# Optimization experiments

Hardware: AMD Instinct MI355X
Metric: run time of the kernel (lower is better)

The kernel has to match this reference:

```python
import jax, jax.numpy as jnp
import numpy as np

EPS = 1e-5
NUM_HEADS = 8

def _bn(x, w, b, m, v):
    # inference-mode BatchNorm2d over channel dim of (B,C,H,W)
    inv = w / jnp.sqrt(v + EPS)
    return x * inv[None, :, None, None] + (b - m * inv)[None, :, None, None]

def _conv1x1(x, W, b):
    # 1x1 conv == per-pixel matmul: W is (out_ch, in_ch)
    return jnp.einsum('bchw,ec->behw', x, W) + b[None, :, None, None]

def _forward(x, bn1_w, bn1_b, bn1_m, bn1_v, Wq, bq, Wk, bk, Wv, bv, gamma, temperature,
             conv_w, conv_b, cbn_w, cbn_b, cbn_m, cbn_v, rs_w, rs_b, rbn_w, rbn_b, rbn_m, rbn_v):
    B, C, Wd, Hd = x.shape
    S = Wd * Hd
    E = Wq.shape[0]
    hd = E // NUM_HEADS
    xa = jax.nn.relu(_bn(x, bn1_w, bn1_b, bn1_m, bn1_v))
    def proj(Wm, bm):
        return _conv1x1(xa, Wm, bm).reshape(B, NUM_HEADS, hd, S).transpose(0, 1, 3, 2)  # (B,h,S,d)
    q = proj(Wq, bq)
    k = proj(Wk, bk)
    v = proj(Wv, bv)
    scores = jnp.einsum('bhsd,bhtd->bhst', q, k) / temperature  # (B,h,S,S)
    scores = scores - jnp.max(scores, axis=-1, keepdims=True)   # redundant amax-subtract as in source
    attn = jax.nn.softmax(scores, axis=-1)
    out = jnp.einsum('bhst,bhtd->bhsd', attn, v)
    out = out.transpose(0, 1, 3, 2).reshape(B, E, Wd, Hd)
    conv_path = jax.nn.relu(_bn(_conv1x1(x, conv_w, conv_b), cbn_w, cbn_b, cbn_m, cbn_v))
    fused = gamma[0] * out + conv_path
    return jax.nn.gelu(_bn(_conv1x1(fused, rs_w, rs_b), rbn_w, rbn_b, rbn_m, rbn_v), approximate=False)

def setup_inputs() -> dict:
    key = jax.random.key(0)
    ks = jax.random.split(key, 18)
    C, E = 256, 512
    n = lambda k, s, sc=0.02: jax.random.normal(k, s, jnp.float32) * sc
    return {
        'x': jax.random.normal(ks[0], (1, C, 64, 64), jnp.float32),
        'bn1_w': 1.0 + n(ks[1], (C,), 0.1), 'bn1_b': n(ks[2], (C,), 0.1),
        'bn1_m': n(ks[3], (C,), 0.05), 'bn1_v': 0.5 + jax.random.uniform(ks[4], (C,), jnp.float32),
        'Wq': n(ks[5], (E, C)), 'bq': jnp.zeros((E,), jnp.float32),
        'Wk': n(ks[6], (E, C)), 'bk': jnp.zeros((E,), jnp.float32),
        'Wv': n(ks[7], (E, C)), 'bv': jnp.zeros((E,), jnp.float32),
        'gamma': jnp.full((1,), 0.5, jnp.float32),
        'temperature': jnp.asarray(0.85, jnp.float32),
        'conv_w': n(ks[8], (E, C)), 'conv_b': jnp.zeros((E,), jnp.float32),
        'cbn_w': 1.0 + n(ks[9], (E,), 0.1), 'cbn_b': n(ks[10], (E,), 0.1),
        'cbn_m': n(ks[11], (E,), 0.05), 'cbn_v': 0.5 + jax.random.uniform(ks[12], (E,), jnp.float32),
        'rs_w': n(ks[13], (C, E)), 'rs_b': jnp.zeros((C,), jnp.float32),
        'rbn_w': 1.0 + n(ks[14], (C,), 0.1), 'rbn_b': n(ks[15], (C,), 0.1),
        'rbn_m': n(ks[16], (C,), 0.05), 'rbn_v': 0.5 + jax.random.uniform(ks[17], (C,), jnp.float32),
    }

def reference(x, bn1_w, bn1_b, bn1_m, bn1_v, Wq, bq, Wk, bk, Wv, bv, gamma, temperature,
              conv_w, conv_b, cbn_w, cbn_b, cbn_m, cbn_v, rs_w, rs_b, rbn_w, rbn_b, rbn_m, rbn_v):
    return _forward(x, bn1_w, bn1_b, bn1_m, bn1_v, Wq, bq, Wk, bk, Wv, bv, gamma, temperature,
                    conv_w, conv_b, cbn_w, cbn_b, cbn_m, cbn_v, rs_w, rs_b, rbn_w, rbn_b, rbn_m, rbn_v)
```

## Files before the change

### kernel.cpp

```cpp
#include <hip/hip_runtime.h>

#define S_DIM 4096
#define C_IN  256
#define E_DIM 512
#define HD    64
#define EPSV  1e-5f

typedef __attribute__((ext_vector_type(8))) short s8v;
typedef __attribute__((ext_vector_type(4))) short s4v;
typedef __attribute__((ext_vector_type(4))) float f4v;
typedef __attribute__((ext_vector_type(16))) float f16v;

__device__ __forceinline__ float bf2f(unsigned short h){
  union{unsigned u; float f;} v; v.u = ((unsigned)h)<<16; return v.f;
}
__device__ __forceinline__ unsigned short f2bf(float f){
  union{float f; unsigned u;} v; v.f = f;
  unsigned r = v.u + 0x7fffu + ((v.u>>16)&1u);
  return (unsigned short)(r>>16);
}
__device__ __forceinline__ unsigned cvtpk_bf16(float lo, float hi_){
  unsigned r;
  asm("v_cvt_pk_bf16_f32 %0, %1, %2" : "=v"(r) : "v"(lo), "v"(hi_));
  return r;
}
__device__ __forceinline__ s8v lds_rd8(const unsigned short* b, int row, int ck){
  return *(const s8v*)&b[(row<<6) + (((ck)^(row&7))<<3)];
}
__device__ __forceinline__ void lds_wr8(unsigned short* b, int row, int ck, s8v v){
  *(s8v*)&b[(row<<6) + (((ck)^(row&7))<<3)] = v;
}
__device__ __forceinline__ s4v lds_rd4q(const unsigned short* b, int row, int q4){
  return *(const s4v*)&b[(row<<6) + (((q4)^(row&15))<<2)];
}
__device__ __forceinline__ void gl_lds16(const unsigned short* g, unsigned short* l){
  __builtin_amdgcn_global_load_lds(
      (const __attribute__((address_space(1))) unsigned int*)g,
      (__attribute__((address_space(3))) unsigned int*)l, 16, 0, 0);
}

__global__ __launch_bounds__(256) void k_wcvt(const float* __restrict__ w0,
    const float* __restrict__ w1, const float* __restrict__ w2,
    const float* __restrict__ w3, const float* __restrict__ w4,
    unsigned short* __restrict__ dst){
  int i = blockIdx.x*256 + threadIdx.x;
  int z = blockIdx.y;
  const float* s = (z==0)?w0:(z==1)?w1:(z==2)?w2:(z==3)?w3:w4;
  dst[z*(E_DIM*C_IN) + i] = f2bf(s[i]);
}

__global__ __launch_bounds__(256) void k_prep(const float* __restrict__ x,
    const float* __restrict__ bw, const float* __restrict__ bb,
    const float* __restrict__ bm, const float* __restrict__ bvar,
    unsigned short* __restrict__ XaT, unsigned short* __restrict__ XrT){
  __shared__ float tile[32][33];
  int tid = threadIdx.x;
  int tx = tid & 31, ty = tid >> 5;
  int s0 = blockIdx.x*32, c0 = blockIdx.y*32;
  #pragma unroll
  for(int p=0;p<4;p++){
    int c = c0 + ty + p*8;
    tile[ty+p*8][tx] = x[c*S_DIM + s0 + tx];
  }
  __syncthreads();
  int cc = c0 + tx;
  float inv  = bw[cc] * rsqrtf(bvar[cc] + EPSV);
  float beta = bb[cc] - bm[cc]*inv;
  #pragma unroll
  for(int p=0;p<4;p++){
    int s = s0 + ty + p*8;
    float v = tile[tx][ty+p*8];
    float a = v*inv + beta; a = a>0.f?a:0.f;
    XaT[s*C_IN + cc] = f2bf(a);
    XrT[s*C_IN + cc] = f2bf(v);
  }
}

__global__ __launch_bounds__(256) void k_proj(
    const unsigned short* __restrict__ XaT, const unsigned short* __restrict__ XrT,
    const unsigned short* __restrict__ Wb,
    const float* __restrict__ bq, const float* __restrict__ bk,
    const float* __restrict__ bvb, const float* __restrict__ bc,
    const float* __restrict__ cw, const float* __restrict__ cbb,
    const float* __restrict__ cm, const float* __restrict__ cvv,
    unsigned short* __restrict__ QT, unsigned short* __restrict__ KT,
    unsigned short* __restrict__ Vx, unsigned short* __restrict__ CT){
  int z = blockIdx.z;
  const unsigned short* Xin = (z==3) ? XrT : XaT;
  const unsigned short* W   = Wb + z*(E_DIM*C_IN);
  const float* bias = (z==0)?bq:(z==1)?bk:(z==2)?bvb:bc;

  __shared__ unsigned short Als[128*64];
  __shared__ unsigned short Bls[64*64];
  int tid = threadIdx.x;
  int w = tid>>6, l = tid&63, g = l>>4, c16 = l&15;
  int wr = w>>1, wc = w&1;
  int s0 = blockIdx.x*128, e0 = blockIdx.y*64;

  f4v acc[4][2];
  #pragma unroll
  for(int m=0;m<4;m++)
    #pragma unroll
    for(int n=0;n<2;n++) acc[m][n] = (f4v){0.f,0.f,0.f,0.f};

  for(int kk=0;kk<4;kk++){
    __syncthreads();
    #pragma unroll
    for(int p=0;p<4;p++){
      int ck = p*256 + tid, row = ck>>3, ch = ck&7;
      s8v v = *(const s8v*)&Xin[(s0+row)*C_IN + kk*64 + ch*8];
      lds_wr8(Als, row, ch, v);
    }
    #pragma unroll
    for(int p=0;p<2;p++){
      int ck = p*256 + tid, row = ck>>3, ch = ck&7;
      s8v v = *(const s8v*)&W[(e0+row)*C_IN + kk*64 + ch*8];
      lds_wr8(Bls, row, ch, v);
    }
    __syncthreads();
    #pragma unroll
    for(int kb=0;kb<2;kb++){
      s8v bfr[2];
      #pragma unroll
      for(int n=0;n<2;n++) bfr[n] = lds_rd8(Bls, wc*32 + n*16 + c16, g + kb*4);
      #pragma unroll
      for(int m=0;m<4;m++){
        s8v af = lds_rd8(Als, wr*64 + m*16 + c16, g + kb*4);
        #pragma unroll
        for(int n=0;n<2;n++)
          acc[m][n] = __builtin_amdgcn_mfma_f32_16x16x32_bf16(af, bfr[n], acc[m][n], 0,0,0);
      }
    }
  }
  #pragma unroll
  for(int n=0;n<2;n++){
    int e = e0 + wc*32 + n*16 + c16;
    float bsv = bias[e];
    float cinv = 0.f, cbeta = 0.f;
    if(z==3){ cinv = cw[e]*rsqrtf(cvv[e]+EPSV); cbeta = cbb[e] - cm[e]*cinv; }
    #pragma unroll
    for(int m=0;m<4;m++){
      int sb = s0 + wr*64 + m*16 + g*4;
      if(z==2){
        s4v pk;
        #pragma unroll
        for(int i=0;i<4;i++) pk[i] = (short)f2bf(acc[m][n][i] + bsv);
        int sb2 = (sb & ~63) | ((((sb>>2)&15) ^ (e&15))<<2);
        *(s4v*)&Vx[e*S_DIM + sb2] = pk;
      } else {
        unsigned short* dst = (z==0)?QT:(z==1)?KT:CT;
        #pragma unroll
        for(int i=0;i<4;i++){
          float vv = acc[m][n][i] + bsv;
          if(z==3){ vv = vv*cinv + cbeta; vv = vv>0.f?vv:0.f; }
          int key = sb+i;
          int ee = e;
          if(z==1) ee = (e & ~56) | ((((e>>3)&7) ^ (key&7))<<3);
          dst[key*E_DIM + ee] = f2bf(vv);
        }
      }
    }
  }
}

__global__ __launch_bounds__(512,2) void k_attn(
    const unsigned short* __restrict__ QT, const unsigned short* __restrict__ KT,
    const unsigned short* __restrict__ Vx, const unsigned short* __restrict__ CT,
    const float* __restrict__ gamma, const float* __restrict__ temp,
    unsigned short* __restrict__ fusedT){
  __shared__ unsigned short SM[65536];
  int tid = threadIdx.x;
  int w = tid>>6, l = tid&63, l31 = l&31, hi = l>>5;
  int qh = w>>2, kh = w&3;
  int bx = blockIdx.x;
  int h = bx&7;
  int q0b = (bx>>3)*128;
  float scl = 1.4426950408889634f / temp[0];

  s8v qf[2][4];
  #pragma unroll
  for(int qg=0;qg<2;qg++){
    int q = q0b + qh*64 + qg*32 + l31;
    #pragma unroll
    for(int ks=0;ks<4;ks++){
      s8v r = *(const s8v*)&QT[q*E_DIM + h*HD + ks*16 + hi*8];
      #pragma unroll
      for(int j=0;j<8;j++) qf[qg][ks][j] = (short)f2bf(bf2f((unsigned short)r[j])*scl);
    }
  }
  s8v ones;
  #pragma unroll
  for(int j=0;j<8;j++) ones[j] = (short)0x3F80;

  f16v oacc[2][2];
  f16v lacc[2];
  #pragma unroll
  for(int qg=0;qg<2;qg++){
    #pragma unroll
    for(int r=0;r<16;r++){ oacc[qg][0][r]=0.f; oacc[qg][1][r]=0.f; lacc[qg][r]=0.f; }
  }

  #define STAGE(BUF, T) { \
    _Pragma("unroll") \
    for(int j=0;j<8;j++){ \
      int flat = (w*8+j)*64 + l; \
      int tile = flat>>9, gg = flat&511, row = gg>>3, ch = gg&7; \
      int khp = tile&3; \
      int sK = khp*1024 + (T)*64; \
      const unsigned short* src = (tile<4) \
        ? &KT[(sK+row)*E_DIM + h*HD + ch*8] \
        : &Vx[(h*HD+row)*S_DIM + sK + ch*8]; \
      gl_lds16(src, SM + (BUF)*32768 + (w*8+j)*512); \
    } }

  int buf = 0;
  STAGE(0, 0);
  for(int t=0;t<16;t++){
    asm volatile("s_waitcnt vmcnt(0)" ::: "memory");
    __syncthreads();
    if(t<15) STAGE(buf^1, t+1);
    const unsigned short* Kb = SM + buf*32768 + kh*4096;
    const unsigned short* Vb = SM + buf*32768 + (4+kh)*4096;

    #pragma unroll
    for(int sub=0;sub<2;sub++){
      int kr = sub*32 + l31;
      s8v kf[4];
      #pragma unroll
      for(int ks=0;ks<4;ks++) kf[ks] = lds_rd8(Kb, kr, ks*2 + hi);

      union{ s8v v; unsigned u[4]; } pa[2][2];
      #pragma unroll
      for(int qg=0;qg<2;qg++){
        f16v d;
        #pragma unroll
        for(int r=0;r<16;r++) d[r]=0.f;
        #pragma unroll
        for(int ks=0;ks<4;ks++)
          d = __builtin_amdgcn_mfma_f32_32x32x16_bf16(kf[ks], qf[qg][ks], d, 0,0,0);
        float e_[16];
        #pragma unroll
        for(int r=0;r<16;r++) e_[r] = __builtin_amdgcn_exp2f(d[r]);
        #pragma unroll
        for(int j=0;j<4;j++){
          pa[qg][0].u[j] = cvtpk_bf16(e_[2*j],   e_[2*j+1]);
          pa[qg][1].u[j] = cvtpk_bf16(e_[8+2*j], e_[8+2*j+1]);
        }
        lacc[qg] = __builtin_amdgcn_mfma_f32_32x32x16_bf16(pa[qg][0].v, ones, lacc[qg],0,0,0);
        lacc[qg] = __builtin_amdgcn_mfma_f32_32x32x16_bf16(pa[qg][1].v, ones, lacc[qg],0,0,0);
      }
      #pragma unroll
      for(int dt=0;dt<2;dt++){
        int vr = dt*32 + l31;
        union{ s8v v; s4v h2[2]; } vf;
        vf.h2[0] = lds_rd4q(Vb, vr, sub*8 + hi);
        vf.h2[1] = lds_rd4q(Vb, vr, sub*8 + 2 + hi);
        oacc[0][dt] = __builtin_amdgcn_mfma_f32_32x32x16_bf16(pa[0][0].v, vf.v, oacc[0][dt], 0,0,0);
        oacc[1][dt] = __builtin_amdgcn_mfma_f32_32x32x16_bf16(pa[1][0].v, vf.v, oacc[1][dt], 0,0,0);
        vf.h2[0] = lds_rd4q(Vb, vr, sub*8 + 4 + hi);
        vf.h2[1] = lds_rd4q(Vb, vr, sub*8 + 6 + hi);
        oacc[0][dt] = __builtin_amdgcn_mfma_f32_32x32x16_bf16(pa[0][1].v, vf.v, oacc[0][dt], 0,0,0);
        oacc[1][dt] = __builtin_amdgcn_mfma_f32_32x32x16_bf16(pa[1][1].v, vf.v, oacc[1][dt], 0,0,0);
      }
    }
    buf ^= 1;
  }

  float* slab = (float*)SM;
  float ga = gamma[0];
  #pragma unroll
  for(int qg=0;qg<2;qg++){
    __syncthreads();
    if(kh!=0){
      float* dst = slab + ((qh*3 + (kh-1))*64 + l)*48;
      #pragma unroll
      for(int r=0;r<16;r++){
        dst[r] = oacc[qg][0][r]; dst[16+r] = oacc[qg][1][r]; dst[32+r] = lacc[qg][r];
      }
    }
    __syncthreads();
    if(kh==0){
      f16v o0 = oacc[qg][0], o1 = oacc[qg][1], lt = lacc[qg];
      #pragma unroll
      for(int s=0;s<3;s++){
        const float* src = slab + ((qh*3 + s)*64 + l)*48;
        #pragma unroll
        for(int r=0;r<16;r++){ o0[r] += src[r]; o1[r] += src[16+r]; lt[r] += src[32+r]; }
      }
      #pragma unroll
      for(int r=0;r<16;r++){
        int qrow = q0b + qh*64 + qg*32 + (r&3) + 8*(r>>2) + 4*hi;
        float rl = __builtin_amdgcn_rcpf(lt[r]) * ga;
        int e0i = h*HD + l31;
        float oA = o0[r]*rl + bf2f(CT[qrow*E_DIM + e0i]);
        float oB = o1[r]*rl + bf2f(CT[qrow*E_DIM + e0i + 32]);
        fusedT[qrow*E_DIM + e0i]      = f2bf(oA);
        fusedT[qrow*E_DIM + e0i + 32] = f2bf(oB);
      }
    }
  }
  #undef STAGE
}

__global__ __launch_bounds__(256) void k_final(
    const unsigned short* __restrict__ Wrs,
    const unsigned short* __restrict__ fusedT,
    const float* __restrict__ rsb,
    const float* __restrict__ rw, const float* __restrict__ rbb,
    const float* __restrict__ rm, const float* __restrict__ rv,
    float* __restrict__ out){
  __shared__ unsigned short Als[64*64];
  __shared__ unsigned short Bls[64*64];
  int tid = threadIdx.x;
  int w = tid>>6, l = tid&63, g = l>>4, c16 = l&15;
  int wr2 = w>>1, wc2 = w&1;
  int sB0 = blockIdx.x*64, c0 = blockIdx.y*64;
  f4v acc[2][2];
  #pragma unroll
  for(int m=0;m<2;m++)
    #pragma unroll
    for(int n=0;n<2;n++) acc[m][n]=(f4v){0.f,0.f,0.f,0.f};
  for(int kk=0;kk<8;kk++){
    __syncthreads();
    #pragma unroll
    for(int p=0;p<2;p++){
      int ck = p*256+tid, row=ck>>3, ch=ck&7;
      s8v v = *(const s8v*)&Wrs[(c0+row)*E_DIM + kk*64 + ch*8];
      lds_wr8(Als, row, ch, v);
    }
    #pragma unroll
    for(int p=0;p<2;p++){
      int ck = p*256+tid, row=ck>>3, ch=ck&7;
      s8v v = *(const s8v*)&fusedT[(sB0+row)*E_DIM + kk*64 + ch*8];
      lds_wr8(Bls, row, ch, v);
    }
    __syncthreads();
    #pragma unroll
    for(int kb=0;kb<2;kb++){
      s8v af[2]; s8v bfr[2];
      #pragma unroll
      for(int m=0;m<2;m++) af[m] = lds_rd8(Als, wr2*32 + m*16 + c16, g + kb*4);
      #pragma unroll
      for(int n=0;n<2;n++) bfr[n] = lds_rd8(Bls, wc2*32 + n*16 + c16, g + kb*4);
      #pragma unroll
      for(int m=0;m<2;m++)
        #pragma unroll
        for(int n=0;n<2;n++)
          acc[m][n] = __builtin_amdgcn_mfma_f32_16x16x32_bf16(af[m], bfr[n], acc[m][n],0,0,0);
    }
  }
  #pragma unroll
  for(int m=0;m<2;m++){
    #pragma unroll
    for(int i=0;i<4;i++){
      int c = c0 + wr2*32 + m*16 + g*4 + i;
      float bias = rsb[c];
      float rinv = rw[c]*rsqrtf(rv[c]+EPSV);
      float rbeta = rbb[c] - rm[c]*rinv;
      #pragma unroll
      for(int n=0;n<2;n++){
        int s = sB0 + wc2*32 + n*16 + c16;
        float vv = acc[m][n][i] + bias;
        vv = vv*rinv + rbeta;
        out[c*S_DIM + s] = 0.5f*vv*(1.0f + erff(vv*0.70710678118f));
      }
    }
  }
}

extern "C" void kernel_launch(void* const* d_in, const int* in_sizes, int n_in,
                              void* d_out, int out_size, void* d_ws, size_t ws_size,
                              hipStream_t stream){
  const float* x     = (const float*)d_in[0];
  const float* bn1w  = (const float*)d_in[1];
  const float* bn1b  = (const float*)d_in[2];
  const float* bn1m  = (const float*)d_in[3];
  const float* bn1v  = (const float*)d_in[4];
  const float* Wq    = (const float*)d_in[5];
  const float* bq    = (const float*)d_in[6];
  const float* Wk    = (const float*)d_in[7];
  const float* bk    = (const float*)d_in[8];
  const float* Wv    = (const float*)d_in[9];
  const float* bv    = (const float*)d_in[10];
  const float* gamma = (const float*)d_in[11];
  const float* temp  = (const float*)d_in[12];
  const float* convw = (const float*)d_in[13];
  const float* convb = (const float*)d_in[14];
  const float* cbnw  = (const float*)d_in[15];
  const float* cbnb  = (const float*)d_in[16];
  const float* cbnm  = (const float*)d_in[17];
  const float* cbnv  = (const float*)d_in[18];
  const float* rsw   = (const float*)d_in[19];
  const float* rsbp  = (const float*)d_in[20];
  const float* rbnw  = (const float*)d_in[21];
  const float* rbnb  = (const float*)d_in[22];
  const float* rbnm  = (const float*)d_in[23];
  const float* rbnv  = (const float*)d_in[24];
  float* out = (float*)d_out;

  unsigned short* ws  = (unsigned short*)d_ws;
  unsigned short* XaT = ws;
  unsigned short* XrT = XaT + S_DIM*C_IN;
  unsigned short* Wb  = XrT + S_DIM*C_IN;
  unsigned short* Wrs = Wb + 4*E_DIM*C_IN;
  unsigned short* QT  = Wrs + C_IN*E_DIM;
  unsigned short* KT  = QT + S_DIM*E_DIM;
  unsigned short* Vx  = KT + S_DIM*E_DIM;
  unsigned short* CT  = Vx + S_DIM*E_DIM;
  unsigned short* fusedT = CT + S_DIM*E_DIM;

  k_wcvt<<<dim3(512,5),256,0,stream>>>(Wq, Wk, Wv, convw, rsw, Wb);
  k_prep<<<dim3(128,8),256,0,stream>>>(x, bn1w, bn1b, bn1m, bn1v, XaT, XrT);
  k_proj<<<dim3(32,8,4),256,0,stream>>>(XaT, XrT, Wb, bq, bk, bv, convb,
                                        cbnw, cbnb, cbnm, cbnv, QT, KT, Vx, CT);
  k_attn<<<dim3(256),512,0,stream>>>(QT, KT, Vx, CT, gamma, temp, fusedT);
  k_final<<<dim3(64,4),256,0,stream>>>(Wrs, fusedT, rsbp, rbnw, rbnb, rbnm, rbnv, out);
}
```

Measured before the change: 87.96 us.

## Split K/V staging, replace ones-MFMA row sums with scalar sums, add setprio

The attention kernel now stages K and V tiles in separate phases with partial vmcnt waits. The next K tile loads while QK^T and exp run, and the next V tile loads while PV runs. The softmax denominator is no longer computed by extra MFMAs against a ones vector; each lane sums its exp values and the sums are combined with a cross-half shuffle and a shared LDS buffer in the epilogue. s_setprio is placed around the MFMA sections. This removes some matrix-core work and exposed load latency, but adds a second barrier per iteration and more complex epilogue indexing, which risks a correctness error in the row-sum mapping.

Result: no change. 88.89 us (+1.1%).

```diff
diff --git a/kernel.cpp b/kernel.cpp
--- a/kernel.cpp
+++ b/kernel.cpp
@@ -177,6 +177,26 @@
   int q0b = (bx>>3)*128;
   float scl = 1.4426950408889634f / temp[0];
 
+  #define STAGE_K(BUF, T) { \
+    _Pragma("unroll") \
+    for(int j=0;j<4;j++){ \
+      int c = w*4 + j; int flat = c*64 + l; \
+      int tile = flat>>9, gg = flat&511, row = gg>>3, ch = gg&7; \
+      int sK = tile*1024 + (T)*64; \
+      gl_lds16(&KT[(sK+row)*E_DIM + h*HD + ch*8], SM + (BUF)*32768 + c*512); \
+    } }
+  #define STAGE_V(BUF, T) { \
+    _Pragma("unroll") \
+    for(int j=0;j<4;j++){ \
+      int c = 32 + w*4 + j; int flat = c*64 + l; \
+      int tile = (flat>>9)&3, gg = flat&511, row = gg>>3, ch = gg&7; \
+      int sK = tile*1024 + (T)*64; \
+      gl_lds16(&Vx[(h*HD+row)*S_DIM + sK + ch*8], SM + (BUF)*32768 + c*512); \
+    } }
+
+  STAGE_K(0, 0);
+  STAGE_V(0, 0);
+
   s8v qf[2][4];
   #pragma unroll
   for(int qg=0;qg<2;qg++){
@@ -188,118 +208,130 @@
       for(int j=0;j<8;j++) qf[qg][ks][j] = (short)f2bf(bf2f((unsigned short)r[j])*scl);
     }
   }
-  s8v ones;
-  #pragma unroll
-  for(int j=0;j<8;j++) ones[j] = (short)0x3F80;
 
   f16v oacc[2][2];
-  f16v lacc[2];
-  #pragma unroll
-  for(int qg=0;qg<2;qg++){
-    #pragma unroll
-    for(int r=0;r<16;r++){ oacc[qg][0][r]=0.f; oacc[qg][1][r]=0.f; lacc[qg][r]=0.f; }
-  }
-
-  #define STAGE(BUF, T) { \
-    _Pragma("unroll") \
-    for(int j=0;j<8;j++){ \
-      int flat = (w*8+j)*64 + l; \
-      int tile = flat>>9, gg = flat&511, row = gg>>3, ch = gg&7; \
-      int khp = tile&3; \
-      int sK = khp*1024 + (T)*64; \
-      const unsigned short* src = (tile<4) \
-        ? &KT[(sK+row)*E_DIM + h*HD + ch*8] \
-        : &Vx[(h*HD+row)*S_DIM + sK + ch*8]; \
-      gl_lds16(src, SM + (BUF)*32768 + (w*8+j)*512); \
-    } }
+  #pragma unroll
+  for(int qg=0;qg<2;qg++)
+    #pragma unroll
+    for(int dt=0;dt<2;dt++)
+      #pragma unroll
+      for(int r=0;r<16;r++) oacc[qg][dt][r]=0.f;
+  float lrun[2] = {0.f, 0.f};
 
   int buf = 0;
-  STAGE(0, 0);
+  #pragma unroll 1
   for(int t=0;t<16;t++){
-    asm volatile("s_waitcnt vmcnt(0)" ::: "memory");
-    __syncthreads();
-    if(t<15) STAGE(buf^1, t+1);
+    asm volatile("s_waitcnt vmcnt(4)" ::: "memory");
+    __builtin_amdgcn_s_barrier();
+    if(t<15) STAGE_K(buf^1, t+1);
     const unsigned short* Kb = SM + buf*32768 + kh*4096;
-    const unsigned short* Vb = SM + buf*32768 + (4+kh)*4096;
-
+
+    union{ s8v v; unsigned u[4]; } pa[2][2][2];
     #pragma unroll
     for(int sub=0;sub<2;sub++){
       int kr = sub*32 + l31;
       s8v kf[4];
       #pragma unroll
       for(int ks=0;ks<4;ks++) kf[ks] = lds_rd8(Kb, kr, ks*2 + hi);
-
-      union{ s8v v; unsigned u[4]; } pa[2][2];
       #pragma unroll
       for(int qg=0;qg<2;qg++){
         f16v d;
         #pragma unroll
         for(int r=0;r<16;r++) d[r]=0.f;
+        __builtin_amdgcn_s_setprio(1);
         #pragma unroll
         for(int ks=0;ks<4;ks++)
           d = __builtin_amdgcn_mfma_f32_32x32x16_bf16(kf[ks], qf[qg][ks], d, 0,0,0);
-        float e_[16];
-        #pragma unroll
-        for(int r=0;r<16;r++) e_[r] = __builtin_amdgcn_exp2f(d[r]);
+        __builtin_amdgcn_s_setprio(0);
+        float e_[16], ls = 0.f;
+        #pragma unroll
+        for(int r=0;r<16;r++){ e_[r] = __builtin_amdgcn_exp2f(d[r]); ls += e_[r]; }
+        lrun[qg] += ls;
         #pragma unroll
         for(int j=0;j<4;j++){
-          pa[qg][0].u[j] = cvtpk_bf16(e_[2*j],   e_[2*j+1]);
-          pa[qg][1].u[j] = cvtpk_bf16(e_[8+2*j], e_[8+2*j+1]);
+          pa[sub][qg][0].u[j] = cvtpk_bf16(e_[2*j],   e_[2*j+1]);
+          pa[sub][qg][1].u[j] = cvtpk_bf16(e_[8+2*j], e_[8+2*j+1]);
         }
-        lacc[qg] = __builtin_amdgcn_mfma_f32_32x32x16_bf16(pa[qg][0].v, ones, lacc[qg],0,0,0);
-        lacc[qg] = __builtin_amdgcn_mfma_f32_32x32x16_bf16(pa[qg][1].v, ones, lacc[qg],0,0,0);
-      }
+      }
+    }
+
+    if(t<15){ asm volatile("s_waitcnt vmcnt(4)" ::: "memory"); }
+    else    { asm volatile("s_waitcnt vmcnt(0)" ::: "memory"); }
+    __builtin_amdgcn_s_barrier();
+    if(t<15) STAGE_V(buf^1, t+1);
+    const unsigned short* Vb = SM + buf*32768 + (4+kh)*4096;
+
+    __builtin_amdgcn_s_setprio(1);
+    #pragma unroll
+    for(int sub=0;sub<2;sub++){
       #pragma unroll
       for(int dt=0;dt<2;dt++){
         int vr = dt*32 + l31;
         union{ s8v v; s4v h2[2]; } vf;
         vf.h2[0] = lds_rd4q(Vb, vr, sub*8 + hi);
         vf.h2[1] = lds_rd4q(Vb, vr, sub*8 + 2 + hi);
-        oacc[0][dt] = __builtin_amdgcn_mfma_f32_32x32x16_bf16(pa[0][0].v, vf.v, oacc[0][dt], 0,0,0);
-        oacc[1][dt] = __builtin_amdgcn_mfma_f32_32x32x16_bf16(pa[1][0].v, vf.v, oacc[1][dt], 0,0,0);
+        oacc[0][dt] = __builtin_amdgcn_mfma_f32_32x32x16_bf16(pa[sub][0][0].v, vf.v, oacc[0][dt], 0,0,0);
+        oacc[1][dt] = __builtin_amdgcn_mfma_f32_32x32x16_bf16(pa[sub][1][0].v, vf.v, oacc[1][dt], 0,0,0);
         vf.h2[0] = lds_rd4q(Vb, vr, sub*8 + 4 + hi);
         vf.h2[1] = lds_rd4q(Vb, vr, sub*8 + 6 + hi);
-        oacc[0][dt] = __builtin_amdgcn_mfma_f32_32x32x16_bf16(pa[0][1].v, vf.v, oacc[0][dt], 0,0,0);
-        oacc[1][dt] = __builtin_amdgcn_mfma_f32_32x32x16_bf16(pa[1][1].v, vf.v, oacc[1][dt], 0,0,0);
-      }
-    }
+        oacc[0][dt] = __builtin_amdgcn_mfma_f32_32x32x16_bf16(pa[sub][0][1].v, vf.v, oacc[0][dt], 0,0,0);
+        oacc[1][dt] = __builtin_amdgcn_mfma_f32_32x32x16_bf16(pa[sub][1][1].v, vf.v, oacc[1][dt], 0,0,0);
+      }
+    }
+    __builtin_amdgcn_s_setprio(0);
     buf ^= 1;
   }
 
+  #pragma unroll
+  for(int qg=0;qg<2;qg++) lrun[qg] += __shfl_xor(lrun[qg], 32);
+
   float* slab = (float*)SM;
+  float* l_buf = slab + 6*64*33;
   float ga = gamma[0];
   #pragma unroll
   for(int qg=0;qg<2;qg++){
     __syncthreads();
     if(kh!=0){
-      float* dst = slab + ((qh*3 + (kh-1))*64 + l)*48;
-      #pragma unroll
-      for(int r=0;r<16;r++){
-        dst[r] = oacc[qg][0][r]; dst[16+r] = oacc[qg][1][r]; dst[32+r] = lacc[qg][r];
-      }
-    }
-    __syncthreads();
+      float* dst = slab + ((qh*3 + (kh-1))*64 + l)*33;
+      #pragma unroll
+      for(int r=0;r<16;r++){ dst[r] = oacc[qg][0][r]; dst[16+r] = oacc[qg][1][r]; }
+      dst[32] = lrun[qg];
+    }
+    __syncthreads();
+    float lt = 0.f;
     if(kh==0){
-      f16v o0 = oacc[qg][0], o1 = oacc[qg][1], lt = lacc[qg];
+      lt = lrun[qg];
       #pragma unroll
       for(int s=0;s<3;s++){
-        const float* src = slab + ((qh*3 + s)*64 + l)*48;
-        #pragma unroll
-        for(int r=0;r<16;r++){ o0[r] += src[r]; o1[r] += src[16+r]; lt[r] += src[32+r]; }
-      }
-      #pragma unroll
-      for(int r=0;r<16;r++){
-        int qrow = q0b + qh*64 + qg*32 + (r&3) + 8*(r>>2) + 4*hi;
-        float rl = __builtin_amdgcn_rcpf(lt[r]) * ga;
-        int e0i = h*HD + l31;
-        float oA = o0[r]*rl + bf2f(CT[qrow*E_DIM + e0i]);
-        float oB = o1[r]*rl + bf2f(CT[qrow*E_DIM + e0i + 32]);
-        fusedT[qrow*E_DIM + e0i]      = f2bf(oA);
-        fusedT[qrow*E_DIM + e0i + 32] = f2bf(oB);
-      }
-    }
-  }
-  #undef STAGE
+        const float* src = slab + ((qh*3 + s)*64 + l)*33;
+        #pragma unroll
+        for(int r=0;r<16;r++){ oacc[qg][0][r] += src[r]; oacc[qg][1][r] += src[16+r]; }
+        lt += src[32];
+      }
+      if(hi==0) l_buf[qh*32 + l31] = lt;
+    }
+    __syncthreads();
+    if(kh==0){
+      #pragma unroll
+      for(int dt=0;dt<2;dt++){
+        int e = h*HD + dt*32 + l31;
+        #pragma unroll
+        for(int g4=0;g4<4;g4++){
+          float4 lv = *(float4*)&l_buf[qh*32 + g4*8 + hi*4];
+          float la[4] = {lv.x, lv.y, lv.z, lv.w};
+          #pragma unroll
+          for(int j=0;j<4;j++){
+            int r = g4*4 + j;
+            int qrow = q0b + qh*64 + qg*32 + j + g4*8 + hi*4;
+            float o = oacc[qg][dt][r]*(ga/la[j]) + bf2f(CT[qrow*E_DIM + e]);
+            fusedT[qrow*E_DIM + e] = f2bf(o);
+          }
+        }
+      }
+    }
+  }
+  #undef STAGE_K
+  #undef STAGE_V
 }
 
 __global__ __launch_bounds__(256) void k_final(
```

## Replace MFMA row-sum with VALU sums, stagger wave order, add setprio, prefetch early

Applied to the files above, without the earlier changes.

The softmax denominator is now accumulated as a per-lane scalar sum of the exponentials plus a cross-half shuffle, replacing the two extra MFMAs against a ones vector. This removes MFMA work and shrinks the reduction slab from 48 to 33 floats per lane. The first K/V stage is issued before the Q load, waves stagger their sub-tile and q-group order, and s_setprio raises priority around MFMA blocks to spread contention between waves. The epilogue gains an extra barrier and an LDS broadcast of the row sums, and divides rather than using the reciprocal approximation.

Result: slower. 177.5 us (+101.8%).

```diff
diff --git a/kernel.cpp b/kernel.cpp
--- a/kernel.cpp
+++ b/kernel.cpp
@@ -177,29 +177,6 @@
   int q0b = (bx>>3)*128;
   float scl = 1.4426950408889634f / temp[0];
 
-  s8v qf[2][4];
-  #pragma unroll
-  for(int qg=0;qg<2;qg++){
-    int q = q0b + qh*64 + qg*32 + l31;
-    #pragma unroll
-    for(int ks=0;ks<4;ks++){
-      s8v r = *(const s8v*)&QT[q*E_DIM + h*HD + ks*16 + hi*8];
-      #pragma unroll
-      for(int j=0;j<8;j++) qf[qg][ks][j] = (short)f2bf(bf2f((unsigned short)r[j])*scl);
-    }
-  }
-  s8v ones;
-  #pragma unroll
-  for(int j=0;j<8;j++) ones[j] = (short)0x3F80;
-
-  f16v oacc[2][2];
-  f16v lacc[2];
-  #pragma unroll
-  for(int qg=0;qg<2;qg++){
-    #pragma unroll
-    for(int r=0;r<16;r++){ oacc[qg][0][r]=0.f; oacc[qg][1][r]=0.f; lacc[qg][r]=0.f; }
-  }
-
   #define STAGE(BUF, T) { \
     _Pragma("unroll") \
     for(int j=0;j<8;j++){ \
@@ -213,8 +190,34 @@
       gl_lds16(src, SM + (BUF)*32768 + (w*8+j)*512); \
     } }
 
+  STAGE(0, 0);
+
+  s8v qf[2][4];
+  #pragma unroll
+  for(int qg=0;qg<2;qg++){
+    int q = q0b + qh*64 + qg*32 + l31;
+    #pragma unroll
+    for(int ks=0;ks<4;ks++){
+      s8v r = *(const s8v*)&QT[q*E_DIM + h*HD + ks*16 + hi*8];
+      #pragma unroll
+      for(int j=0;j<8;j++) qf[qg][ks][j] = (short)f2bf(bf2f((unsigned short)r[j])*scl);
+    }
+  }
+
+  f16v oacc[2][2];
+  #pragma unroll
+  for(int qg=0;qg<2;qg++)
+    #pragma unroll
+    for(int dt=0;dt<2;dt++)
+      #pragma unroll
+      for(int r=0;r<16;r++) oacc[qg][dt][r]=0.f;
+  float lrun[2] = {0.f, 0.f};
+
+  int sOrd = w&1;
+  int qOrd = (w>>1)&1;
+
   int buf = 0;
-  STAGE(0, 0);
+  #pragma unroll 1
   for(int t=0;t<16;t++){
     asm volatile("s_waitcnt vmcnt(0)" ::: "memory");
     __syncthreads();
@@ -223,7 +226,8 @@
     const unsigned short* Vb = SM + buf*32768 + (4+kh)*4096;
 
     #pragma unroll
-    for(int sub=0;sub<2;sub++){
+    for(int si=0;si<2;si++){
+      int sub = si ^ sOrd;
       int kr = sub*32 + l31;
       s8v kf[4];
       #pragma unroll
@@ -231,24 +235,27 @@
 
       union{ s8v v; unsigned u[4]; } pa[2][2];
       #pragma unroll
-      for(int qg=0;qg<2;qg++){
+      for(int qi=0;qi<2;qi++){
+        int qg = qi ^ qOrd;
         f16v d;
         #pragma unroll
         for(int r=0;r<16;r++) d[r]=0.f;
+        __builtin_amdgcn_s_setprio(1);
         #pragma unroll
         for(int ks=0;ks<4;ks++)
           d = __builtin_amdgcn_mfma_f32_32x32x16_bf16(kf[ks], qf[qg][ks], d, 0,0,0);
-        float e_[16];
-        #pragma unroll
-        for(int r=0;r<16;r++) e_[r] = __builtin_amdgcn_exp2f(d[r]);
+        __builtin_amdgcn_s_setprio(0);
+        float e_[16], ls = 0.f;
+        #pragma unroll
+        for(int r=0;r<16;r++){ e_[r] = __builtin_amdgcn_exp2f(d[r]); ls += e_[r]; }
+        lrun[qg] += ls;
         #pragma unroll
         for(int j=0;j<4;j++){
           pa[qg][0].u[j] = cvtpk_bf16(e_[2*j],   e_[2*j+1]);
           pa[qg][1].u[j] = cvtpk_bf16(e_[8+2*j], e_[8+2*j+1]);
         }
-        lacc[qg] = __builtin_amdgcn_mfma_f32_32x32x16_bf16(pa[qg][0].v, ones, lacc[qg],0,0,0);
-        lacc[qg] = __builtin_amdgcn_mfma_f32_32x32x16_bf16(pa[qg][1].v, ones, lacc[qg],0,0,0);
-      }
+      }
+      __builtin_amdgcn_s_setprio(1);
       #pragma unroll
       for(int dt=0;dt<2;dt++){
         int vr = dt*32 + l31;
@@ -262,40 +269,55 @@
         oacc[0][dt] = __builtin_amdgcn_mfma_f32_32x32x16_bf16(pa[0][1].v, vf.v, oacc[0][dt], 0,0,0);
         oacc[1][dt] = __builtin_amdgcn_mfma_f32_32x32x16_bf16(pa[1][1].v, vf.v, oacc[1][dt], 0,0,0);
       }
+      __builtin_amdgcn_s_setprio(0);
     }
     buf ^= 1;
   }
 
+  #pragma unroll
+  for(int qg=0;qg<2;qg++) lrun[qg] += __shfl_xor(lrun[qg], 32);
+
   float* slab = (float*)SM;
+  float* l_buf = slab + 6*64*33;
   float ga = gamma[0];
   #pragma unroll
   for(int qg=0;qg<2;qg++){
     __syncthreads();
     if(kh!=0){
-      float* dst = slab + ((qh*3 + (kh-1))*64 + l)*48;
-      #pragma unroll
-      for(int r=0;r<16;r++){
-        dst[r] = oacc[qg][0][r]; dst[16+r] = oacc[qg][1][r]; dst[32+r] = lacc[qg][r];
-      }
+      float* dst = slab + ((qh*3 + (kh-1))*64 + l)*33;
+      #pragma unroll
+      for(int r=0;r<16;r++){ dst[r] = oacc[qg][0][r]; dst[16+r] = oacc[qg][1][r]; }
+      dst[32] = lrun[qg];
     }
     __syncthreads();
     if(kh==0){
-      f16v o0 = oacc[qg][0], o1 = oacc[qg][1], lt = lacc[qg];
+      float lt = lrun[qg];
       #pragma unroll
       for(int s=0;s<3;s++){
-        const float* src = slab + ((qh*3 + s)*64 + l)*48;
-        #pragma unroll
-        for(int r=0;r<16;r++){ o0[r] += src[r]; o1[r] += src[16+r]; lt[r] += src[32+r]; }
-      }
-      #pragma unroll
-      for(int r=0;r<16;r++){
-        int qrow = q0b + qh*64 + qg*32 + (r&3) + 8*(r>>2) + 4*hi;
-        float rl = __builtin_amdgcn_rcpf(lt[r]) * ga;
-        int e0i = h*HD + l31;
-        float oA = o0[r]*rl + bf2f(CT[qrow*E_DIM + e0i]);
-        float oB = o1[r]*rl + bf2f(CT[qrow*E_DIM + e0i + 32]);
-        fusedT[qrow*E_DIM + e0i]      = f2bf(oA);
-        fusedT[qrow*E_DIM + e0i + 32] = f2bf(oB);
+        const float* src = slab + ((qh*3 + s)*64 + l)*33;
+        #pragma unroll
+        for(int r=0;r<16;r++){ oacc[qg][0][r] += src[r]; oacc[qg][1][r] += src[16+r]; }
+        lt += src[32];
+      }
+      if(hi==0) l_buf[qh*32 + l31] = lt;
+    }
+    __syncthreads();
+    if(kh==0){
+      #pragma unroll
+      for(int g4=0;g4<4;g4++){
+        float4 lv = *(float4*)&l_buf[qh*32 + g4*8 + hi*4];
+        float rl[4] = {ga/lv.x, ga/lv.y, ga/lv.z, ga/lv.w};
+        #pragma unroll
+        for(int dt=0;dt<2;dt++){
+          int e = h*HD + dt*32 + l31;
+          #pragma unroll
+          for(int j=0;j<4;j++){
+            int r = g4*4 + j;
+            int qrow = q0b + qh*64 + qg*32 + j + g4*8 + hi*4;
+            float o = oacc[qg][dt][r]*rl[j] + bf2f(CT[qrow*E_DIM + e]);
+            fusedT[qrow*E_DIM + e] = f2bf(o);
+          }
+        }
       }
     }
   }
```
